# Optimization experiments

Measured on AMD Instinct MI355X. Metric: run time of the kernel, lower is better.

The kernel has to match this reference:

```python
import jax, jax.numpy as jnp
import numpy as np


def setup_inputs() -> dict:
    key = jax.random.key(0)
    x = jax.random.normal(key, (8, 4096, 1024), dtype=jnp.float32)
    return {"x": x}


def reference(x) -> jnp.ndarray:
    # Faithful to the flax module: causal mask of zeros/-inf -> softmax ->
    # row i has uniform weights 1/(i+1) over positions 0..i, then attn @ x.
    B, T, C = x.shape
    tril = jnp.tril(jnp.ones((T, T), dtype=jnp.float32))
    attn = jnp.where(tril == 0, -jnp.inf, jnp.zeros((T, T), dtype=jnp.float32))
    attn = jax.nn.softmax(attn, axis=-1)  # [T, T], row i = 1/(i+1) on [0..i]
    # broadcast matmul over batch: [T,T] x [B,T,C] -> [B,T,C]
    return jnp.einsum('ts,bsc->btc', attn, x)
```

## Files before the change

kernel.cpp:

```cpp
#include <hip/hip_runtime.h>
#include <stdint.h>

namespace {

constexpr int kB      = 8;
constexpr int kT      = 4096;
constexpr int kC4     = 256;
constexpr int kSegLen = 64;
constexpr int kNSeg   = kT / kSegLen;
constexpr int kTiles  = kB * kNSeg;
constexpr int kSub    = 16;

constexpr size_t kStOff   = 256;
constexpr size_t kStWords = (size_t)kTiles * 4 * kC4;

typedef float f4 __attribute__((ext_vector_type(4)));

__device__ __forceinline__ uint64_t ld_st(const uint64_t* p) {
    return __hip_atomic_load(p, __ATOMIC_RELAXED, __HIP_MEMORY_SCOPE_AGENT);
}
__device__ __forceinline__ void st_st(uint64_t* p, uint64_t w) {
    __hip_atomic_store(p, w, __ATOMIC_RELAXED, __HIP_MEMORY_SCOPE_AGENT);
}

__global__ __launch_bounds__(1024, 4) void fused_scan(const float4* __restrict__ x,
                                                      float4* __restrict__ out,
                                                      uint32_t* __restrict__ ticket,
                                                      uint64_t* __restrict__ st) {
    __shared__ float4   s_sums[4][kC4];
    __shared__ float4   s_off[kC4];
    __shared__ uint32_t s_tile;

    if (threadIdx.x == 0) s_tile = atomicAdd(ticket, 1u);
    __syncthreads();
    const uint32_t tile = s_tile;
    const int b   = (int)(tile & 7u);
    const int seg = (int)(tile >> 3);
    const int c4  = (int)(threadIdx.x & 255u);
    const int q   = (int)(threadIdx.x >> 8);

    const size_t base = ((size_t)(b * kT + seg * kSegLen + q * kSub)) * kC4 + c4;
    const float4* p = x + base;
    float4 v[kSub];
#pragma unroll
    for (int i = 0; i < kSub; ++i) v[i] = p[(size_t)i * kC4];

    float sx = 0.f, sy = 0.f, sz = 0.f, sw = 0.f;
#pragma unroll
    for (int i = 0; i < kSub; ++i) {
        sx += v[i].x; sy += v[i].y; sz += v[i].z; sw += v[i].w;
    }
    s_sums[q][c4] = make_float4(sx, sy, sz, sw);
    __syncthreads();

    float px = 0.f, py = 0.f, pz = 0.f, pw = 0.f;
    for (int qq = 0; qq < q; ++qq) {
        const float4 s = s_sums[qq][c4];
        px += s.x; py += s.y; pz += s.z; pw += s.w;
    }

    if (q == 3) {
        const float a[4] = { px + sx, py + sy, pz + sz, pw + sw };
#pragma unroll
        for (int j = 0; j < 4; ++j) {
            const size_t idx = ((size_t)((b * kNSeg + seg) * 4 + j) << 8) + c4;
            st_st(st + idx, ((uint64_t)__float_as_uint(a[j]) << 32) | 1u);
        }
    }
    if (q == 0) {
        float ox = 0.f, oy = 0.f, oz = 0.f, ow = 0.f;
        int s = 0;
        while (s < seg) {
            uint64_t w[4][4];
            bool ok = true;
#pragma unroll
            for (int k = 0; k < 4; ++k) {
                const bool in = (s + k) < seg;
#pragma unroll
                for (int j = 0; j < 4; ++j) {
                    const size_t idx =
                        ((size_t)((b * kNSeg + (s + k)) * 4 + j) << 8) + c4;
                    w[k][j] = in ? ld_st(st + idx) : (uint64_t)1u;
                }
            }
#pragma unroll
            for (int k = 0; k < 4; ++k)
#pragma unroll
                for (int j = 0; j < 4; ++j) ok &= ((uint32_t)w[k][j] != 0u);
            if (!ok) { __builtin_amdgcn_s_sleep(2); continue; }
#pragma unroll
            for (int k = 0; k < 4; ++k) {
                ox += __uint_as_float((uint32_t)(w[k][0] >> 32));
                oy += __uint_as_float((uint32_t)(w[k][1] >> 32));
                oz += __uint_as_float((uint32_t)(w[k][2] >> 32));
                ow += __uint_as_float((uint32_t)(w[k][3] >> 32));
            }
            s += 4;
        }
        s_off[c4] = make_float4(ox, oy, oz, ow);
    }
    __syncthreads();

    const float4 co = s_off[c4];
    float ox = co.x + px, oy = co.y + py, oz = co.z + pz, ow = co.w + pw;
    f4* o = (f4*)(out + base);
    const int t0 = seg * kSegLen + q * kSub;
#pragma unroll
    for (int i = 0; i < kSub; ++i) {
        ox += v[i].x; oy += v[i].y; oz += v[i].z; ow += v[i].w;
        const float inv = __builtin_amdgcn_rcpf((float)(t0 + i + 1));
        f4 r;
        r.x = ox * inv; r.y = oy * inv; r.z = oz * inv; r.w = ow * inv;
        __builtin_nontemporal_store(r, o + (size_t)i * kC4);
    }
}

}

extern "C" void kernel_launch(void* const* d_in, const int* in_sizes, int n_in,
                              void* d_out, int out_size, void* d_ws, size_t ws_size,
                              hipStream_t stream) {
    const float4* x = (const float4*)d_in[0];
    float4* out     = (float4*)d_out;
    uint32_t* ctr   = (uint32_t*)d_ws;
    uint64_t* st    = (uint64_t*)((char*)d_ws + kStOff);
    (void)hipMemsetAsync(d_ws, 0, kStOff + kStWords * sizeof(uint64_t), stream);
    fused_scan<<<kTiles, 1024, 0, stream>>>(x, out, ctr, st);
}
```

Before: 72.33 us.

## Switch to decoupled look-back scan with 256-thread tiles of 16 rows

```diff
diff --git a/kernel.cpp b/kernel.cpp
--- a/kernel.cpp
+++ b/kernel.cpp
@@ -3,13 +3,12 @@
 
 namespace {
 
-constexpr int kB      = 8;
-constexpr int kT      = 4096;
-constexpr int kC4     = 256;
-constexpr int kSegLen = 64;
-constexpr int kNSeg   = kT / kSegLen;
-constexpr int kTiles  = kB * kNSeg;
-constexpr int kSub    = 16;
+constexpr int kB       = 8;
+constexpr int kT       = 4096;
+constexpr int kC4      = 256;
+constexpr int kSub     = 16;
+constexpr int kSegPerB = kT / kSub;
+constexpr int kTiles   = kB * kSegPerB;
 
 constexpr size_t kStOff   = 256;
 constexpr size_t kStWords = (size_t)kTiles * 4 * kC4;
@@ -22,89 +21,86 @@
 __device__ __forceinline__ void st_st(uint64_t* p, uint64_t w) {
     __hip_atomic_store(p, w, __ATOMIC_RELAXED, __HIP_MEMORY_SCOPE_AGENT);
 }
+__device__ __forceinline__ size_t sidx(int b, int s, int j, int c4) {
+    return ((size_t)(((((b << 8) | s) << 2) | j)) << 8) | (unsigned)c4;
+}
 
-__global__ __launch_bounds__(1024, 4) void fused_scan(const float4* __restrict__ x,
-                                                      float4* __restrict__ out,
-                                                      uint32_t* __restrict__ ticket,
-                                                      uint64_t* __restrict__ st) {
-    __shared__ float4   s_sums[4][kC4];
-    __shared__ float4   s_off[kC4];
+__global__ __launch_bounds__(256, 4) void lb_scan(const float4* __restrict__ x,
+                                                  float4* __restrict__ out,
+                                                  uint32_t* __restrict__ ticket,
+                                                  uint64_t* __restrict__ st) {
     __shared__ uint32_t s_tile;
-
     if (threadIdx.x == 0) s_tile = atomicAdd(ticket, 1u);
     __syncthreads();
     const uint32_t tile = s_tile;
     const int b   = (int)(tile & 7u);
     const int seg = (int)(tile >> 3);
-    const int c4  = (int)(threadIdx.x & 255u);
-    const int q   = (int)(threadIdx.x >> 8);
+    const int c4  = (int)threadIdx.x;
 
-    const size_t base = ((size_t)(b * kT + seg * kSegLen + q * kSub)) * kC4 + c4;
+    const size_t base = ((size_t)(b * kT + seg * kSub)) * kC4 + c4;
     const float4* p = x + base;
     float4 v[kSub];
 #pragma unroll
     for (int i = 0; i < kSub; ++i) v[i] = p[(size_t)i * kC4];
-
-    float sx = 0.f, sy = 0.f, sz = 0.f, sw = 0.f;
+    float ax = 0.f, ay = 0.f, az = 0.f, aw = 0.f;
 #pragma unroll
     for (int i = 0; i < kSub; ++i) {
-        sx += v[i].x; sy += v[i].y; sz += v[i].z; sw += v[i].w;
-    }
-    s_sums[q][c4] = make_float4(sx, sy, sz, sw);
-    __syncthreads();
-
-    float px = 0.f, py = 0.f, pz = 0.f, pw = 0.f;
-    for (int qq = 0; qq < q; ++qq) {
-        const float4 s = s_sums[qq][c4];
-        px += s.x; py += s.y; pz += s.z; pw += s.w;
+        ax += v[i].x; ay += v[i].y; az += v[i].z; aw += v[i].w;
     }
 
-    if (q == 3) {
-        const float a[4] = { px + sx, py + sy, pz + sz, pw + sw };
+    {
+        const uint32_t tag = (seg == 0) ? 2u : 1u;
+        const float a[4] = { ax, ay, az, aw };
 #pragma unroll
-        for (int j = 0; j < 4; ++j) {
-            const size_t idx = ((size_t)((b * kNSeg + seg) * 4 + j) << 8) + c4;
-            st_st(st + idx, ((uint64_t)__float_as_uint(a[j]) << 32) | 1u);
-        }
+        for (int j = 0; j < 4; ++j)
+            st_st(st + sidx(b, seg, j, c4),
+                  ((uint64_t)__float_as_uint(a[j]) << 32) | tag);
     }
-    if (q == 0) {
-        float ox = 0.f, oy = 0.f, oz = 0.f, ow = 0.f;
-        int s = 0;
-        while (s < seg) {
+
+    float rx = 0.f, ry = 0.f, rz = 0.f, rw = 0.f;
+    if (seg > 0) {
+        bool done[4] = { false, false, false, false };
+        float run[4] = { 0.f, 0.f, 0.f, 0.f };
+        int s = seg - 1;
+        while (!(done[0] && done[1] && done[2] && done[3])) {
             uint64_t w[4][4];
             bool ok = true;
 #pragma unroll
             for (int k = 0; k < 4; ++k) {
-                const bool in = (s + k) < seg;
+                const int  sk = s - k;
+                const bool in = sk >= 0;
 #pragma unroll
-                for (int j = 0; j < 4; ++j) {
-                    const size_t idx =
-                        ((size_t)((b * kNSeg + (s + k)) * 4 + j) << 8) + c4;
-                    w[k][j] = in ? ld_st(st + idx) : (uint64_t)1u;
-                }
+                for (int j = 0; j < 4; ++j)
+                    w[k][j] = in ? ld_st(st + sidx(b, sk, j, c4)) : (uint64_t)2u;
             }
 #pragma unroll
             for (int k = 0; k < 4; ++k)
 #pragma unroll
                 for (int j = 0; j < 4; ++j) ok &= ((uint32_t)w[k][j] != 0u);
-            if (!ok) { __builtin_amdgcn_s_sleep(2); continue; }
+            if (!ok) { __builtin_amdgcn_s_sleep(4); continue; }
 #pragma unroll
             for (int k = 0; k < 4; ++k) {
-                ox += __uint_as_float((uint32_t)(w[k][0] >> 32));
-                oy += __uint_as_float((uint32_t)(w[k][1] >> 32));
-                oz += __uint_as_float((uint32_t)(w[k][2] >> 32));
-                ow += __uint_as_float((uint32_t)(w[k][3] >> 32));
+#pragma unroll
+                for (int j = 0; j < 4; ++j) {
+                    if (!done[j]) {
+                        run[j] += __uint_as_float((uint32_t)(w[k][j] >> 32));
+                        done[j] = ((uint32_t)w[k][j] == 2u);
+                    }
+                }
             }
-            s += 4;
+            s -= 4;
         }
-        s_off[c4] = make_float4(ox, oy, oz, ow);
+        rx = run[0]; ry = run[1]; rz = run[2]; rw = run[3];
+        const float pr[4] = { rx + ax, ry + ay, rz + az, rw + aw };
+#pragma unroll
+        for (int j = 0; j < 4; ++j)
+            st_st(st + sidx(b, seg, j, c4),
+                  ((uint64_t)__float_as_uint(pr[j]) << 32) | 2u);
     }
-    __syncthreads();
 
-    const float4 co = s_off[c4];
-    float ox = co.x + px, oy = co.y + py, oz = co.z + pz, ow = co.w + pw;
     f4* o = (f4*)(out + base);
-    const int t0 = seg * kSegLen + q * kSub;
+    const int t0 = seg * kSub;
+    float ox = rx, oy = ry, oz = rz, ow = rw;
 #pragma unroll
     for (int i = 0; i < kSub; ++i) {
         ox += v[i].x; oy += v[i].y; oz += v[i].z; ow += v[i].w;
@@ -125,5 +121,5 @@
     uint32_t* ctr   = (uint32_t*)d_ws;
     uint64_t* st    = (uint64_t*)((char*)d_ws + kStOff);
     (void)hipMemsetAsync(d_ws, 0, kStOff + kStWords * sizeof(uint64_t), stream);
-    fused_scan<<<kTiles, 1024, 0, stream>>>(x, out, ctr, st);
+    lb_scan<<<kTiles, 256, 0, stream>>>(x, out, ctr, st);
 }
```

Result: slower. 135.8 us (+87.7%).
